# Kernel optimization log

Hardware: AMD Instinct MI355X
Metric: run time of the kernel (lower is better)

The kernel has to match this reference:

```python
import jax, jax.numpy as jnp
import numpy as np

# Block-sparse causal local attention (DeepSpeed SparseSelfAttention math):
#   scores = SDD(Q, K^T) on nonzero layout blocks
#   scores = masked_fill(block-causal mask == 0, -inf)
#   probs  = sparse_softmax(scores * head_dim**-0.5)  (rpe=None, key_padding_mask=None)
#   out    = DSD(probs, V)
# Layout: block (i, j) is nonzero iff 0 <= i - j < W (causal sliding window of W blocks).

BSZ, H, S, D = 2, 8, 4096, 64
BLK = 32          # sparsity block size
W = 16            # number of local key blocks per query block (512-token window)


def setup_inputs() -> dict:
    key = jax.random.key(0)
    kq, kk, kv = jax.random.split(key, 3)
    query = jax.random.normal(kq, (BSZ, H, S, D), jnp.float32)
    k = jax.random.normal(kk, (BSZ, H, S, D), jnp.float32)
    v = jax.random.normal(kv, (BSZ, H, S, D), jnp.float32)
    return {"query": query, "key": k, "value": v}


def reference(query, key, value):
    b, h, s, d = query.shape
    nb = s // BLK
    scaling = float(d) ** -0.5

    qb = query.reshape(b, h, nb, BLK, d)
    kb = key.reshape(b, h, nb, BLK, d)
    vb = value.reshape(b, h, nb, BLK, d)

    blk_i = jnp.arange(nb)
    # key-block indices attended by each query block: i-W+1 ... i   [nb, W]
    k_idx = blk_i[:, None] + jnp.arange(-(W - 1), 1)[None, :]
    blk_valid = k_idx >= 0
    k_idx_c = jnp.maximum(k_idx, 0)

    Kg = kb[:, :, k_idx_c]   # [b, h, nb, W, BLK, d]
    Vg = vb[:, :, k_idx_c]   # [b, h, nb, W, BLK, d]

    # block-sparse SDD: only the W local blocks per query block are computed
    scores = jnp.einsum('bhnqd,bhnwkd->bhnqwk', qb, Kg) * scaling

    # token-level causal mask (covers the diagonal-block triangular mask
    # from make_sparse_attn_mask) + validity of gathered blocks
    qpos = blk_i[:, None] * BLK + jnp.arange(BLK)[None, :]           # [nb, BLK]
    kpos = k_idx_c[..., None] * BLK + jnp.arange(BLK)                # [nb, W, BLK]
    allowed = blk_valid[:, None, :, None] & (kpos[:, None, :, :] <= qpos[:, :, None, None])
    scores = jnp.where(allowed[None, None], scores, -jnp.inf)

    # fused sparse softmax over all present key positions of each query row
    probs = jax.nn.softmax(scores.reshape(b, h, nb, BLK, W * BLK), axis=-1)
    probs = probs.reshape(b, h, nb, BLK, W, BLK)

    # block-sparse DSD
    out = jnp.einsum('bhnqwk,bhnwkd->bhnqd', probs, Vg)
    return out.reshape(b, h, s, d)
```

## Files before the change

### kernel.cpp

```cpp
#include <hip/hip_runtime.h>
#include <hip/hip_bf16.h>


#define NH    8
#define SEQ   4096
#define DIM   64
#define NBLK  128
#define WIN   16
#define QG    4
#define GROUPS (NBLK / QG)

typedef __bf16 bf16x8 __attribute__((ext_vector_type(8)));
typedef __bf16 bf16x4 __attribute__((ext_vector_type(4)));
typedef float  f32x4  __attribute__((ext_vector_type(4)));
typedef float  f32x2  __attribute__((ext_vector_type(2)));
typedef unsigned short u16;
typedef unsigned int   u32;

#define KSTR 72
#define VSTR 40
#define M0   12.0f

__device__ __forceinline__ bf16x4 cvt4(f32x4 a) {
    bf16x4 r;
#pragma unroll
    for (int j = 0; j < 4; ++j) r[j] = (__bf16)a[j];
    return r;
}

__global__ __launch_bounds__(512)
void sparse_attn_v21(const float* __restrict__ Q,
                     const float* __restrict__ K,
                     const float* __restrict__ V,
                     float* __restrict__ O)
{
    const int b  = (int)blockIdx.x;
    const int lg = (b & 7) * 64 + (b >> 3);
    const int bh = lg >> 5;
    const int n0 = (lg & 31) * QG;

    const int t    = (int)threadIdx.x;
    const int wave = t >> 6;
    const int lane = t & 63;
    const int l15  = lane & 15;
    const int l4   = lane >> 4;
    const int qi   = wave >> 1;
    const int rh   = wave & 1;
    const int nq   = n0 + qi;

    __shared__ u16 Kt[2][32][KSTR];
    __shared__ u16 Vt[2][64][VSTR];

    const size_t base = (size_t)bh * SEQ * DIM;
    const float SC = 0.125f * 1.44269504088896340736f;

    const int skrow = t >> 4;
    const int skc   = (t & 15) * 4;
    const int svkey = (t & 15) * 2;
    const int svd2  = t >> 4;
    const int vp    = (svkey & 3) | (((svkey >> 2) & 3) << 3) | ((svkey >> 4) << 2);

    bf16x8 qf[2];
    {
        const float* qp = Q + base + (size_t)(nq * 32 + rh * 16 + l15) * DIM + l4 * 8;
        f32x4 a0 = *(const f32x4*)qp        * SC;
        f32x4 b0 = *(const f32x4*)(qp + 4)  * SC;
        f32x4 a1 = *(const f32x4*)(qp + 32) * SC;
        f32x4 b1 = *(const f32x4*)(qp + 36) * SC;
#pragma unroll
        for (int j = 0; j < 4; ++j) {
            qf[0][j] = (__bf16)a0[j]; qf[0][4 + j] = (__bf16)b0[j];
            qf[1][j] = (__bf16)a1[j]; qf[1][4 + j] = (__bf16)b1[j];
        }
    }

    bf16x8 onesf;
#pragma unroll
    for (int j = 0; j < 8; ++j) onesf[j] = (__bf16)1.0f;

    f32x4 acc[4] = {};
    f32x4 accl = {};

    const int lo  = (nq >= WIN - 1) ? nq - (WIN - 1) : 0;
    const int kb0 = (n0 >= WIN - 1) ? n0 - (WIN - 1) : 0;
    const int kb1 = n0 + QG - 1;

    f32x4 kr;  f32x2 va, vb;
    {
        const float* kp = K + base + (size_t)(kb0 * 32 + skrow) * DIM + skc;
        kr = *(const f32x4*)kp;
        const float* vptr = V + base + (size_t)(kb0 * 32 + svkey) * DIM + svd2 * 2;
        va = *(const f32x2*)vptr;
        vb = *(const f32x2*)(vptr + DIM);
    }
    {
        *(bf16x4*)&Kt[0][skrow][skc] = cvt4(kr);
#pragma unroll
        for (int j = 0; j < 2; ++j) {
            u32 w = (u32)__builtin_bit_cast(u16, (__bf16)va[j])
                  | ((u32)__builtin_bit_cast(u16, (__bf16)vb[j]) << 16);
            *(u32*)&Vt[0][svd2 * 2 + j][vp] = w;
        }
    }
    __syncthreads();

    int cur = 0;
    for (int kb = kb0; kb <= kb1; ++kb) {
        {
            const int kn = (kb + 1 <= kb1) ? kb + 1 : kb1;
            const float* kp = K + base + (size_t)(kn * 32 + skrow) * DIM + skc;
            kr = *(const f32x4*)kp;
            const float* vptr = V + base + (size_t)(kn * 32 + svkey) * DIM + svd2 * 2;
            va = *(const f32x2*)vptr;
            vb = *(const f32x2*)(vptr + DIM);
        }

        if (kb >= lo && kb <= nq) {
            bf16x8 kf[2][2];
#pragma unroll
            for (int kh = 0; kh < 2; ++kh)
#pragma unroll
                for (int c = 0; c < 2; ++c)
                    kf[kh][c] = *(const bf16x8*)&Kt[cur][kh * 16 + l15][c * 32 + l4 * 8];

            bf16x8 vf[4];
#pragma unroll
            for (int dt = 0; dt < 4; ++dt)
                vf[dt] = *(const bf16x8*)&Vt[cur][dt * 16 + l15][l4 * 8];

            f32x4 s[2];
#pragma unroll
            for (int kh = 0; kh < 2; ++kh) {
                f32x4 a = {};
                a = __builtin_amdgcn_mfma_f32_16x16x32_bf16(kf[kh][0], qf[0], a, 0, 0, 0);
                a = __builtin_amdgcn_mfma_f32_16x16x32_bf16(kf[kh][1], qf[1], a, 0, 0, 0);
                s[kh] = a;
            }

            if (kb == nq) {
#pragma unroll
                for (int kh = 0; kh < 2; ++kh)
#pragma unroll
                    for (int r = 0; r < 4; ++r)
                        if (kh * 16 + l4 * 4 + r > rh * 16 + l15)
                            s[kh][r] = -1e30f;
            }

            bf16x8 pbf;
#pragma unroll
            for (int j = 0; j < 8; ++j)
                pbf[j] = (__bf16)exp2f(s[j >> 2][j & 3] - M0);

#pragma unroll
            for (int dt = 0; dt < 4; ++dt)
                acc[dt] = __builtin_amdgcn_mfma_f32_16x16x32_bf16(
                    vf[dt], pbf, acc[dt], 0, 0, 0);
            accl = __builtin_amdgcn_mfma_f32_16x16x32_bf16(onesf, pbf, accl, 0, 0, 0);
        }

        {
            *(bf16x4*)&Kt[cur ^ 1][skrow][skc] = cvt4(kr);
#pragma unroll
            for (int j = 0; j < 2; ++j) {
                u32 w = (u32)__builtin_bit_cast(u16, (__bf16)va[j])
                      | ((u32)__builtin_bit_cast(u16, (__bf16)vb[j]) << 16);
                *(u32*)&Vt[cur ^ 1][svd2 * 2 + j][vp] = w;
            }
        }

        __syncthreads();
        cur ^= 1;
    }

    {
        const float inv = 1.0f / accl[0];
        float* op = O + base + (size_t)(nq * 32 + rh * 16 + l15) * DIM + l4 * 4;
#pragma unroll
        for (int dt = 0; dt < 4; ++dt) {
            f32x4 v;
#pragma unroll
            for (int r = 0; r < 4; ++r) v[r] = acc[dt][r] * inv;
            *(f32x4*)(op + dt * 16) = v;
        }
    }
}

extern "C" void kernel_launch(void* const* d_in, const int* in_sizes, int n_in,
                              void* d_out, int out_size, void* d_ws, size_t ws_size,
                              hipStream_t stream)
{
    const float* Q = (const float*)d_in[0];
    const float* K = (const float*)d_in[1];
    const float* V = (const float*)d_in[2];
    float*       O = (float*)d_out;

    const int nwg = 2 * NH * GROUPS;
    hipLaunchKernelGGL(sparse_attn_v21, dim3(nwg), dim3(512), 0, stream,
                       Q, K, V, O);
}
```

Baseline: 32.88 us.

## Widen query group to 8 blocks per workgroup, one query block per wave

Each workgroup now handles 8 query blocks instead of 4, and each wave owns a full 32-row query block (two 16-row tiles) instead of half of one. The shared K/V window staged per workgroup now serves twice as many query blocks, which cuts redundant global K/V loads and conversions (the staged range grows from 19 to 23 key blocks for 8 query blocks). In exchange the grid halves to 256 workgroups, which may underfill the GPU, and each wave holds more accumulators and Q fragments, raising register pressure and serialising more MFMA work per wave.

```diff
diff --git a/kernel.cpp b/kernel.cpp
--- a/kernel.cpp
+++ b/kernel.cpp
@@ -7,7 +7,7 @@
 #define DIM   64
 #define NBLK  128
 #define WIN   16
-#define QG    4
+#define QG    8
 #define GROUPS (NBLK / QG)
 
 typedef __bf16 bf16x8 __attribute__((ext_vector_type(8)));
@@ -29,24 +29,22 @@
 }
 
 __global__ __launch_bounds__(512)
-void sparse_attn_v21(const float* __restrict__ Q,
+void sparse_attn_v22(const float* __restrict__ Q,
                      const float* __restrict__ K,
                      const float* __restrict__ V,
                      float* __restrict__ O)
 {
     const int b  = (int)blockIdx.x;
-    const int lg = (b & 7) * 64 + (b >> 3);
-    const int bh = lg >> 5;
-    const int n0 = (lg & 31) * QG;
+    const int lg = (b & 7) * 32 + (b >> 3);
+    const int bh = lg >> 4;
+    const int n0 = (lg & 15) * QG;
 
     const int t    = (int)threadIdx.x;
     const int wave = t >> 6;
     const int lane = t & 63;
     const int l15  = lane & 15;
     const int l4   = lane >> 4;
-    const int qi   = wave >> 1;
-    const int rh   = wave & 1;
-    const int nq   = n0 + qi;
+    const int nq   = n0 + wave;
 
     __shared__ u16 Kt[2][32][KSTR];
     __shared__ u16 Vt[2][64][VSTR];
@@ -60,17 +58,18 @@
     const int svd2  = t >> 4;
     const int vp    = (svkey & 3) | (((svkey >> 2) & 3) << 3) | ((svkey >> 4) << 2);
 
-    bf16x8 qf[2];
-    {
-        const float* qp = Q + base + (size_t)(nq * 32 + rh * 16 + l15) * DIM + l4 * 8;
+    bf16x8 qf[2][2];
+#pragma unroll
+    for (int rt = 0; rt < 2; ++rt) {
+        const float* qp = Q + base + (size_t)(nq * 32 + rt * 16 + l15) * DIM + l4 * 8;
         f32x4 a0 = *(const f32x4*)qp        * SC;
         f32x4 b0 = *(const f32x4*)(qp + 4)  * SC;
         f32x4 a1 = *(const f32x4*)(qp + 32) * SC;
         f32x4 b1 = *(const f32x4*)(qp + 36) * SC;
 #pragma unroll
         for (int j = 0; j < 4; ++j) {
-            qf[0][j] = (__bf16)a0[j]; qf[0][4 + j] = (__bf16)b0[j];
-            qf[1][j] = (__bf16)a1[j]; qf[1][4 + j] = (__bf16)b1[j];
+            qf[rt][0][j] = (__bf16)a0[j]; qf[rt][0][4 + j] = (__bf16)b0[j];
+            qf[rt][1][j] = (__bf16)a1[j]; qf[rt][1][4 + j] = (__bf16)b1[j];
         }
     }
 
@@ -78,8 +77,8 @@
 #pragma unroll
     for (int j = 0; j < 8; ++j) onesf[j] = (__bf16)1.0f;
 
-    f32x4 acc[4] = {};
-    f32x4 accl = {};
+    f32x4 acc[2][4] = {};
+    f32x4 accl[2] = {};
 
     const int lo  = (nq >= WIN - 1) ? nq - (WIN - 1) : 0;
     const int kb0 = (n0 >= WIN - 1) ? n0 - (WIN - 1) : 0;
@@ -128,34 +127,38 @@
             for (int dt = 0; dt < 4; ++dt)
                 vf[dt] = *(const bf16x8*)&Vt[cur][dt * 16 + l15][l4 * 8];
 
-            f32x4 s[2];
-#pragma unroll
-            for (int kh = 0; kh < 2; ++kh) {
-                f32x4 a = {};
-                a = __builtin_amdgcn_mfma_f32_16x16x32_bf16(kf[kh][0], qf[0], a, 0, 0, 0);
-                a = __builtin_amdgcn_mfma_f32_16x16x32_bf16(kf[kh][1], qf[1], a, 0, 0, 0);
-                s[kh] = a;
+#pragma unroll
+            for (int rt = 0; rt < 2; ++rt) {
+                f32x4 s[2];
+#pragma unroll
+                for (int kh = 0; kh < 2; ++kh) {
+                    f32x4 a = {};
+                    a = __builtin_amdgcn_mfma_f32_16x16x32_bf16(kf[kh][0], qf[rt][0], a, 0, 0, 0);
+                    a = __builtin_amdgcn_mfma_f32_16x16x32_bf16(kf[kh][1], qf[rt][1], a, 0, 0, 0);
+                    s[kh] = a;
+                }
+
+                if (kb == nq) {
+#pragma unroll
+                    for (int kh = 0; kh < 2; ++kh)
+#pragma unroll
+                        for (int r = 0; r < 4; ++r)
+                            if (kh * 16 + l4 * 4 + r > rt * 16 + l15)
+                                s[kh][r] = -1e30f;
+                }
+
+                bf16x8 pbf;
+#pragma unroll
+                for (int j = 0; j < 8; ++j)
+                    pbf[j] = (__bf16)exp2f(s[j >> 2][j & 3] - M0);
+
+#pragma unroll
+                for (int dt = 0; dt < 4; ++dt)
+                    acc[rt][dt] = __builtin_amdgcn_mfma_f32_16x16x32_bf16(
+                        vf[dt], pbf, acc[rt][dt], 0, 0, 0);
+                accl[rt] = __builtin_amdgcn_mfma_f32_16x16x32_bf16(
+                    onesf, pbf, accl[rt], 0, 0, 0);
             }
-
-            if (kb == nq) {
-#pragma unroll
-                for (int kh = 0; kh < 2; ++kh)
-#pragma unroll
-                    for (int r = 0; r < 4; ++r)
-                        if (kh * 16 + l4 * 4 + r > rh * 16 + l15)
-                            s[kh][r] = -1e30f;
-            }
-
-            bf16x8 pbf;
-#pragma unroll
-            for (int j = 0; j < 8; ++j)
-                pbf[j] = (__bf16)exp2f(s[j >> 2][j & 3] - M0);
-
-#pragma unroll
-            for (int dt = 0; dt < 4; ++dt)
-                acc[dt] = __builtin_amdgcn_mfma_f32_16x16x32_bf16(
-                    vf[dt], pbf, acc[dt], 0, 0, 0);
-            accl = __builtin_amdgcn_mfma_f32_16x16x32_bf16(onesf, pbf, accl, 0, 0, 0);
         }
 
         {
@@ -172,14 +175,15 @@
         cur ^= 1;
     }
 
-    {
-        const float inv = 1.0f / accl[0];
-        float* op = O + base + (size_t)(nq * 32 + rh * 16 + l15) * DIM + l4 * 4;
+#pragma unroll
+    for (int rt = 0; rt < 2; ++rt) {
+        const float inv = 1.0f / accl[rt][0];
+        float* op = O + base + (size_t)(nq * 32 + rt * 16 + l15) * DIM + l4 * 4;
 #pragma unroll
         for (int dt = 0; dt < 4; ++dt) {
             f32x4 v;
 #pragma unroll
-            for (int r = 0; r < 4; ++r) v[r] = acc[dt][r] * inv;
+            for (int r = 0; r < 4; ++r) v[r] = acc[rt][dt][r] * inv;
             *(f32x4*)(op + dt * 16) = v;
         }
     }
@@ -195,6 +199,6 @@
     float*       O = (float*)d_out;
 
     const int nwg = 2 * NH * GROUPS;
-    hipLaunchKernelGGL(sparse_attn_v21, dim3(nwg), dim3(512), 0, stream,
+    hipLaunchKernelGGL(sparse_attn_v22, dim3(nwg), dim3(512), 0, stream,
                        Q, K, V, O);
 }
```

Result: slower. 34.45 us (+4.8%).

## Precast K/V to bf16 in workspace and read directly from global in attention

Applied to the files above, without the earlier changes.

Adds a prep kernel that converts K to bf16 and V to a transposed bf16 layout in the workspace. The attention kernel then loads MFMA fragments straight from global memory, with no LDS staging and no barriers, and each 4-wave block handles both 16-row halves of a query block. This removes the per-tile fp32->bf16 conversion and the __syncthreads from the main loop. In exchange it adds a second launch and an extra round trip through global memory, and the fallback path needs a large enough workspace.

```diff
diff --git a/kernel.cpp b/kernel.cpp
--- a/kernel.cpp
+++ b/kernel.cpp
@@ -7,8 +7,6 @@
 #define DIM   64
 #define NBLK  128
 #define WIN   16
-#define QG    4
-#define GROUPS (NBLK / QG)
 
 typedef __bf16 bf16x8 __attribute__((ext_vector_type(8)));
 typedef __bf16 bf16x4 __attribute__((ext_vector_type(4)));
@@ -17,9 +15,177 @@
 typedef unsigned short u16;
 typedef unsigned int   u32;
 
+#define M0 12.0f
+
+__device__ __forceinline__ bf16x8 cvt8(f32x4 a, f32x4 b) {
+    bf16x8 r;
+#pragma unroll
+    for (int j = 0; j < 4; ++j) { r[j] = (__bf16)a[j]; r[4 + j] = (__bf16)b[j]; }
+    return r;
+}
+
+#define PVSTR 40
+__global__ __launch_bounds__(256)
+void prep_kernel(const float* __restrict__ K, const float* __restrict__ V,
+                 u16* __restrict__ Kb, u16* __restrict__ Vt)
+{
+    const int wg = (int)blockIdx.x;
+    const int bh = wg >> 7;
+    const int kb = wg & 127;
+    const int t  = (int)threadIdx.x;
+
+    const size_t base = (size_t)bh * SEQ * DIM;
+
+    {
+        const int row = t >> 3;
+        const int c   = (t & 7) * 8;
+        const float* kp = K + base + (size_t)(kb * 32 + row) * DIM + c;
+        bf16x8 o = cvt8(*(const f32x4*)kp, *(const f32x4*)(kp + 4));
+        *(bf16x8*)&Kb[base + (size_t)(kb * 32 + row) * DIM + c] = o;
+    }
+
+    __shared__ u16 Vl[DIM][PVSTR];
+    {
+        const int svkey = (t & 15) * 2;
+        const int svdg  = t >> 4;
+        const float* vp = V + base + (size_t)(kb * 32 + svkey) * DIM + svdg * 4;
+        f32x4 va = *(const f32x4*)vp;
+        f32x4 vb = *(const f32x4*)(vp + DIM);
+#pragma unroll
+        for (int j = 0; j < 4; ++j) {
+            u32 w = (u32)__builtin_bit_cast(u16, (__bf16)va[j])
+                  | ((u32)__builtin_bit_cast(u16, (__bf16)vb[j]) << 16);
+            *(u32*)&Vl[svdg * 4 + j][svkey] = w;
+        }
+    }
+    __syncthreads();
+    {
+        const int d    = t >> 2;
+        const int kseg = (t & 3) * 8;
+        u32 w0 = *(const u32*)&Vl[d][kseg];
+        u32 w1 = *(const u32*)&Vl[d][kseg + 2];
+        u32 w2 = *(const u32*)&Vl[d][kseg + 4];
+        u32 w3 = *(const u32*)&Vl[d][kseg + 6];
+        u32 out[4] = {w0, w1, w2, w3};
+        *(f32x4*)&Vt[(size_t)bh * DIM * SEQ + (size_t)d * SEQ + kb * 32 + kseg] =
+            *(f32x4*)out;
+    }
+}
+
+__global__ __launch_bounds__(256)
+void sparse_attn_v23(const float* __restrict__ Q,
+                     const u16* __restrict__ Kb,
+                     const u16* __restrict__ Vt,
+                     float* __restrict__ O)
+{
+    const int b  = (int)blockIdx.x;
+    const int lg = (b & 7) * 64 + (b >> 3);
+    const int bh = lg >> 5;
+    const int n0 = (lg & 31) * 4;
+
+    const int t    = (int)threadIdx.x;
+    const int wave = t >> 6;
+    const int lane = t & 63;
+    const int l15  = lane & 15;
+    const int l4   = lane >> 4;
+    const int nq   = n0 + wave;
+
+    const size_t base  = (size_t)bh * SEQ * DIM;
+    const size_t vbase = (size_t)bh * DIM * SEQ;
+    const float SC = 0.125f * 1.44269504088896340736f;
+
+    bf16x8 qf[2][2];
+#pragma unroll
+    for (int rt = 0; rt < 2; ++rt) {
+        const float* qp = Q + base + (size_t)(nq * 32 + rt * 16 + l15) * DIM + l4 * 8;
+        f32x4 a0 = *(const f32x4*)qp        * SC;
+        f32x4 b0 = *(const f32x4*)(qp + 4)  * SC;
+        f32x4 a1 = *(const f32x4*)(qp + 32) * SC;
+        f32x4 b1 = *(const f32x4*)(qp + 36) * SC;
+        qf[rt][0] = cvt8(a0, b0);
+        qf[rt][1] = cvt8(a1, b1);
+    }
+
+    bf16x8 onesf;
+#pragma unroll
+    for (int j = 0; j < 8; ++j) onesf[j] = (__bf16)1.0f;
+
+    f32x4 acc[2][4] = {};
+    f32x4 accl[2] = {};
+
+    const int lo = (nq >= WIN - 1) ? nq - (WIN - 1) : 0;
+
+    for (int kb = lo; kb <= nq; ++kb) {
+        bf16x8 kf[2][2];
+#pragma unroll
+        for (int kh = 0; kh < 2; ++kh) {
+            const u16* kp = Kb + base + (size_t)(kb * 32 + kh * 16 + l15) * DIM + l4 * 8;
+            kf[kh][0] = *(const bf16x8*)kp;
+            kf[kh][1] = *(const bf16x8*)(kp + 32);
+        }
+
+        bf16x8 vf[4];
+#pragma unroll
+        for (int dt = 0; dt < 4; ++dt) {
+            const u16* vrow = Vt + vbase + (size_t)(dt * 16 + l15) * SEQ + kb * 32;
+            bf16x4 lo4 = *(const bf16x4*)(vrow + l4 * 4);
+            bf16x4 hi4 = *(const bf16x4*)(vrow + 16 + l4 * 4);
+#pragma unroll
+            for (int j = 0; j < 4; ++j) { vf[dt][j] = lo4[j]; vf[dt][4 + j] = hi4[j]; }
+        }
+
+#pragma unroll
+        for (int rt = 0; rt < 2; ++rt) {
+            f32x4 s[2];
+#pragma unroll
+            for (int kh = 0; kh < 2; ++kh) {
+                f32x4 a = {};
+                a = __builtin_amdgcn_mfma_f32_16x16x32_bf16(kf[kh][0], qf[rt][0], a, 0, 0, 0);
+                a = __builtin_amdgcn_mfma_f32_16x16x32_bf16(kf[kh][1], qf[rt][1], a, 0, 0, 0);
+                s[kh] = a;
+            }
+
+            if (kb == nq) {
+#pragma unroll
+                for (int kh = 0; kh < 2; ++kh)
+#pragma unroll
+                    for (int r = 0; r < 4; ++r)
+                        if (kh * 16 + l4 * 4 + r > rt * 16 + l15)
+                            s[kh][r] = -1e30f;
+            }
+
+            bf16x8 pbf;
+#pragma unroll
+            for (int j = 0; j < 8; ++j)
+                pbf[j] = (__bf16)exp2f(s[j >> 2][j & 3] - M0);
+
+#pragma unroll
+            for (int dt = 0; dt < 4; ++dt)
+                acc[rt][dt] = __builtin_amdgcn_mfma_f32_16x16x32_bf16(
+                    vf[dt], pbf, acc[rt][dt], 0, 0, 0);
+            accl[rt] = __builtin_amdgcn_mfma_f32_16x16x32_bf16(
+                onesf, pbf, accl[rt], 0, 0, 0);
+        }
+    }
+
+#pragma unroll
+    for (int rt = 0; rt < 2; ++rt) {
+        const float inv = 1.0f / accl[rt][0];
+        float* op = O + base + (size_t)(nq * 32 + rt * 16 + l15) * DIM + l4 * 4;
+#pragma unroll
+        for (int dt = 0; dt < 4; ++dt) {
+            f32x4 v;
+#pragma unroll
+            for (int r = 0; r < 4; ++r) v[r] = acc[rt][dt][r] * inv;
+            *(f32x4*)(op + dt * 16) = v;
+        }
+    }
+}
+
+#define QG    4
+#define GROUPS (NBLK / QG)
 #define KSTR 72
 #define VSTR 40
-#define M0   12.0f
 
 __device__ __forceinline__ bf16x4 cvt4(f32x4 a) {
     bf16x4 r;
@@ -194,7 +360,16 @@
     const float* V = (const float*)d_in[2];
     float*       O = (float*)d_out;
 
-    const int nwg = 2 * NH * GROUPS;
-    hipLaunchKernelGGL(sparse_attn_v21, dim3(nwg), dim3(512), 0, stream,
-                       Q, K, V, O);
-}
+    const size_t kb_bytes = (size_t)2 * NH * SEQ * DIM * sizeof(u16);
+    if (ws_size >= 2 * kb_bytes) {
+        u16* Kb = (u16*)d_ws;
+        u16* Vt = (u16*)((char*)d_ws + kb_bytes);
+        hipLaunchKernelGGL(prep_kernel, dim3(2 * NH * NBLK), dim3(256), 0, stream,
+                           K, V, Kb, Vt);
+        hipLaunchKernelGGL(sparse_attn_v23, dim3(512), dim3(256), 0, stream,
+                           Q, Kb, Vt, O);
+    } else {
+        hipLaunchKernelGGL(sparse_attn_v21, dim3(512), dim3(512), 0, stream,
+                           Q, K, V, O);
+    }
+}
```

Result: slower. 65.27 us (+98.5%).
